# Kernel optimization log

Measured on AMD Instinct MI355X. Metric: run time of the kernel, lower is better.

The kernel has to match this reference:

```python
import jax, jax.numpy as jnp
import numpy as np

LAMBD = 0.05

def _mlp(y, W0, b0, W1, b1, W2, b2, W3, b3):
    h = jax.nn.relu(y @ W0.T + b0)
    h = jax.nn.relu(h @ W1.T + b1)
    h = jax.nn.relu(h @ W2.T + b2)
    return h @ W3.T + b3  # [N, 1]


def setup_inputs() -> dict:
    key = jax.random.key(0)
    ks = jax.random.split(key, 8)
    B, N, D = 4096, 20000, 784
    s = lambda fan_in: 1.0 / np.sqrt(fan_in)
    return {
        "x": jax.random.normal(ks[0], (B, D), jnp.float32),
        "y": jax.random.normal(ks[1], (N, D), jnp.float32),
        "nu": jax.random.uniform(ks[2], (N,), jnp.float32, 0.1, 1.0),
        "W0": jax.random.normal(ks[3], (512, D), jnp.float32) * s(D),
        "b0": jnp.zeros((512,), jnp.float32),
        "W1": jax.random.normal(ks[4], (256, 512), jnp.float32) * s(512),
        "b1": jnp.zeros((256,), jnp.float32),
        "W2": jax.random.normal(ks[5], (128, 256), jnp.float32) * s(256),
        "b2": jnp.zeros((128,), jnp.float32),
        "W3": jax.random.normal(ks[6], (1, 128), jnp.float32) * s(128),
        "b3": jnp.zeros((1,), jnp.float32),
    }


def reference(x, y, nu, W0, b0, W1, b1, W2, b2, W3, b3):
    # squared-distance cost matrix [B, N], normalized by mean(|y|^2)
    sy2 = jnp.sum(y * y, axis=1)            # [N]
    normalization = sy2.mean()
    cxy = (jnp.sum(x * x, axis=1, keepdims=True) + sy2[None, :]
           - 2.0 * (x @ y.T)) / normalization  # [B, N]
    psiy = _mlp(y, W0, b0, W1, b1, W2, b2, W3, b3)[:, 0]  # [N]
    # entropic semi-dual: -lambd * logsumexp((psi(y) - c(x,y))/lambd + log nu)
    z = (psiy[None, :] - cxy) / LAMBD + jnp.log(nu)[None, :]
    out = -LAMBD * jax.nn.logsumexp(z, axis=1) + psiy.mean()  # [B]
    return out
```

## Files before the change

### kernel.cpp

```cpp
#include <hip/hip_runtime.h>
#include <math.h>
#include <stdint.h>
#include <stddef.h>

#define B_ROWS 4096
#define N_REAL 20000
#define NP2    20224
#define NJT2   79
#define NRT    16
#define D_IN   784
#define DP2    800
#define NKS    25
#define NKT    13
#define YBLK   316
#define XBLK   64
#define PW     158
#define LAMBD  0.05f
#define LN2    0.69314718055994530942f
#define QS     (4.5f / 127.f)
#define QINV   (127.f / 4.5f)

typedef __attribute__((ext_vector_type(8))) short bf16x8;
typedef __attribute__((ext_vector_type(4))) float f32x4;
typedef __attribute__((ext_vector_type(4))) int   i32x4;

typedef const unsigned int __attribute__((address_space(1)))* gas_u32p;
typedef unsigned int __attribute__((address_space(3)))* las_u32p;

static __device__ __forceinline__ void gload_lds16(const void* g, void* l) {
  __builtin_amdgcn_global_load_lds((gas_u32p)g, (las_u32p)l, 16, 0, 0);
}

static __device__ __forceinline__ float bf2f(short s) {
  union { unsigned u; float f; } c;
  c.u = ((unsigned)(unsigned short)s) << 16;
  return c.f;
}
static __device__ __forceinline__ short f2bf(float f) {
  union { float f; unsigned u; } c;
  c.f = f;
  unsigned r = (c.u + 0x7fffu + ((c.u >> 16) & 1u)) >> 16;
  return (short)(unsigned short)r;
}
static __device__ __forceinline__ unsigned q4c(float a, float b, float c, float d) {
  int x0 = min(127, max(-127, (int)rintf(a * QINV))) & 255;
  int x1 = min(127, max(-127, (int)rintf(b * QINV))) & 255;
  int x2 = min(127, max(-127, (int)rintf(c * QINV))) & 255;
  int x3 = min(127, max(-127, (int)rintf(d * QINV))) & 255;
  return (unsigned)(x0 | (x1 << 8) | (x2 << 16) | (x3 << 24));
}

__global__ void k_prep(const float* __restrict__ ysrc, const float* __restrict__ xsrc,
                       unsigned char* __restrict__ y_i8, unsigned char* __restrict__ x_i8,
                       short* __restrict__ y_bf, float* __restrict__ sy2,
                       float* __restrict__ x2,
                       const float* __restrict__ W0, const float* __restrict__ W1,
                       const float* __restrict__ W2, short* __restrict__ W0b,
                       short* __restrict__ W1b, short* __restrict__ W2b,
                       unsigned* __restrict__ ctr) {
  const int b = blockIdx.x, t = threadIdx.x;
  if (b == 0 && t == 0) *ctr = 0u;

  if (b >= YBLK + XBLK) {
    const int wb_ = b - (YBLK + XBLK);
    const float* src; short* dst; int r, cs, cp;
    if (wb_ < 512)      { r = wb_;       src = W0; dst = W0b; cs = D_IN; cp = DP2; }
    else if (wb_ < 768) { r = wb_ - 512; src = W1; dst = W1b; cs = 512;  cp = 512; }
    else                { r = wb_ - 768; src = W2; dst = W2b; cs = 256;  cp = 256; }
    const float* sp = src + (size_t)r * cs;
    short* dp = dst + (size_t)r * cp;
    for (int c = t; c < cp; c += 256)
      dp[c] = f2bf(c < cs ? sp[c] : 0.f);
    return;
  }

  const float* src; unsigned char* di8; float* rowsum;
  int rows_real, g; bool wbf;
  if (b < YBLK) { src = ysrc; di8 = y_i8; rowsum = sy2;
                  rows_real = N_REAL; g = b; wbf = true; }
  else          { src = xsrc; di8 = x_i8; rowsum = x2;
                  rows_real = B_ROWS; g = b - YBLK; wbf = false; }
  const int q = t & 3, r = t >> 2;
  const int grow = g * 64 + r;
  const int tile1 = grow >> 8, sub1 = grow & 255;
  const float* sp = src + (size_t)grow * D_IN;
  const bool realRow = grow < rows_real;
  float sq = 0.f;

  for (int kt = 0; kt < NKT; ++kt) {
    const int c0 = kt * 64 + q * 16;
    float v[16];
    if (realRow && c0 < D_IN) {
      #pragma unroll
      for (int u = 0; u < 4; ++u) {
        float4 w4 = *(const float4*)(sp + c0 + u * 4);
        v[u*4+0] = w4.x; v[u*4+1] = w4.y; v[u*4+2] = w4.z; v[u*4+3] = w4.w;
        sq += w4.x * w4.x + w4.y * w4.y + w4.z * w4.z + w4.w * w4.w;
      }
    } else {
      #pragma unroll
      for (int e = 0; e < 16; ++e) v[e] = 0.f;
    }
    uint4 pk;
    pk.x = q4c(v[0],  v[1],  v[2],  v[3]);
    pk.y = q4c(v[4],  v[5],  v[6],  v[7]);
    pk.z = q4c(v[8],  v[9],  v[10], v[11]);
    pk.w = q4c(v[12], v[13], v[14], v[15]);
    *(uint4*)(di8 + (size_t)(tile1 * NKT + kt) * 16384
              + ((size_t)(q * 256 + sub1) << 4)) = pk;
    if (wbf) {
      const int ks = kt * 2 + (q >> 1);
      if (ks < NKS) {
        const int oct = (q & 1) * 2;
        short* dp = y_bf + (size_t)(tile1 * NKS + ks) * 8192
                  + ((size_t)(oct * 256 + sub1) << 3);
        bf16x8 o0, o1;
        #pragma unroll
        for (int e = 0; e < 8; ++e) { o0[e] = f2bf(v[e]); o1[e] = f2bf(v[8 + e]); }
        *(bf16x8*)dp = o0;
        *(bf16x8*)(dp + 2048) = o1;
      }
    }
  }

  sq += __shfl_xor(sq, 1, 4);
  sq += __shfl_xor(sq, 2, 4);
  if (q == 0 && realRow) rowsum[grow] = sq;
}

template <bool TA>
__global__ __launch_bounds__(256) void k_gemmf(const short* __restrict__ A,
                                               const short* __restrict__ Bm,
                                               const float* __restrict__ bias,
                                               short* __restrict__ C,
                                               int K, int Ncols,
                                               const float* __restrict__ sy2n,
                                               float* __restrict__ scaln) {
  extern __shared__ short L[];
  const int t = threadIdx.x;
  const int rb = blockIdx.y, cb = blockIdx.x;

  if (sy2n != nullptr && rb == NP2 / 128) {
    if (cb != 0) return;
    __shared__ float red[4];
    float a = 0.f;
    for (int j = t; j < N_REAL; j += 256) a += sy2n[j];
    #pragma unroll
    for (int m = 1; m < 64; m <<= 1) a += __shfl_xor(a, m, 64);
    if ((t & 63) == 0) red[t >> 6] = a;
    __syncthreads();
    if (t == 0) {
      float norm = (red[0] + red[1] + red[2] + red[3]) / (float)N_REAL;
      scaln[0] = norm;
      scaln[1] = 1.0f / norm;
      scaln[2] = 2.0f / (norm * LAMBD * LN2);
    }
    return;
  }

  const int lane = t & 63, wave = t >> 6;
  const int lr = lane & 15, lg = lane >> 4;
  const int wrow = (wave >> 1) * 64, wcol = (wave & 1) * 64;
  const int KS = K >> 5;
  const int wb = wave * 512;

  const int prow = t & 127, psel = t >> 7;
  const short* aS0; const short* aS1; int aStep;
  if constexpr (TA) {
    const short* base = A + (size_t)((rb >> 1) * NKS) * 8192
                      + ((size_t)((rb & 1) * 128 + prow) << 3);
    aS0 = base + (size_t)(psel * 2048);
    aS1 = base + (size_t)((2 + psel) * 2048);
    aStep = 8192;
  } else {
    const short* base = A + (size_t)(rb * 128 + prow) * K;
    aS0 = base + psel * 8;
    aS1 = base + (2 + psel) * 8;
    aStep = 32;
  }
  const short* bBase = Bm + (size_t)(cb * 128 + prow) * K;
  const short* bS0 = bBase + psel * 8;
  const short* bS1 = bBase + (2 + psel) * 8;

  auto stage = [&](int s) {
    short* Lb = L + (s % 3) * 8192;
    gload_lds16(aS0 + (size_t)s * aStep, Lb + wb);
    gload_lds16(aS1 + (size_t)s * aStep, Lb + 2048 + wb);
    gload_lds16(bS0 + (size_t)s * 32,    Lb + 4096 + wb);
    gload_lds16(bS1 + (size_t)s * 32,    Lb + 4096 + 2048 + wb);
  };

  f32x4 acc[4][4];
  #pragma unroll
  for (int mi = 0; mi < 4; ++mi)
    #pragma unroll
    for (int ni = 0; ni < 4; ++ni)
      acc[mi][ni] = (f32x4){0.f, 0.f, 0.f, 0.f};

  stage(0);
  stage(1);
  asm volatile("s_waitcnt vmcnt(4)" ::: "memory");
  __builtin_amdgcn_s_barrier();
  __builtin_amdgcn_sched_barrier(0);

  const int aro = (wrow + lr) * 8;
  const int bro = (wcol + lr) * 8;
  for (int ks = 0; ks < KS; ++ks) {
    if (ks + 2 < KS) stage(ks + 2);
    const short* LA = L + (ks % 3) * 8192 + lg * 1024;
    const short* LB = LA + 4096;
    bf16x8 b0 = *(const bf16x8*)&LB[bro];
    bf16x8 b1 = *(const bf16x8*)&LB[bro + 128];
    bf16x8 b2 = *(const bf16x8*)&LB[bro + 256];
    bf16x8 b3 = *(const bf16x8*)&LB[bro + 384];
    bf16x8 a0 = *(const bf16x8*)&LA[aro];
    bf16x8 a1 = *(const bf16x8*)&LA[aro + 128];
    bf16x8 a2v = *(const bf16x8*)&LA[aro + 256];
    bf16x8 a3v = *(const bf16x8*)&LA[aro + 384];
    __builtin_amdgcn_s_setprio(1);
    #pragma unroll
    for (int ni = 0; ni < 4; ++ni) {
      bf16x8 bv = ni == 0 ? b0 : ni == 1 ? b1 : ni == 2 ? b2 : b3;
      acc[0][ni] = __builtin_amdgcn_mfma_f32_16x16x32_bf16(a0, bv, acc[0][ni], 0, 0, 0);
      acc[1][ni] = __builtin_amdgcn_mfma_f32_16x16x32_bf16(a1, bv, acc[1][ni], 0, 0, 0);
      acc[2][ni] = __builtin_amdgcn_mfma_f32_16x16x32_bf16(a2v, bv, acc[2][ni], 0, 0, 0);
      acc[3][ni] = __builtin_amdgcn_mfma_f32_16x16x32_bf16(a3v, bv, acc[3][ni], 0, 0, 0);
    }
    __builtin_amdgcn_s_setprio(0);
    if (ks + 2 < KS) {
      asm volatile("s_waitcnt vmcnt(4)" ::: "memory");
      __builtin_amdgcn_s_barrier();
      __builtin_amdgcn_sched_barrier(0);
    } else if (ks + 1 < KS) {
      asm volatile("s_waitcnt vmcnt(0)" ::: "memory");
      __builtin_amdgcn_s_barrier();
      __builtin_amdgcn_sched_barrier(0);
    }
  }

  #pragma unroll
  for (int ni = 0; ni < 4; ++ni) {
    const int col = cb * 128 + wcol + ni * 16 + lr;
    const float bv = bias[col];
    #pragma unroll
    for (int mi = 0; mi < 4; ++mi) {
      const int row0 = rb * 128 + wrow + mi * 16 + lg * 4;
      #pragma unroll
      for (int r = 0; r < 4; ++r)
        C[(size_t)(row0 + r) * Ncols + col] = f2bf(fmaxf(acc[mi][ni][r] + bv, 0.f));
    }
  }
}

__global__ __launch_bounds__(256) void k_mlp12(const short* __restrict__ H1,
                                               const short* __restrict__ W1b,
                                               const float* __restrict__ b1,
                                               const short* __restrict__ W2b,
                                               const float* __restrict__ b2,
                                               const float* __restrict__ W3,
                                               const float* __restrict__ b3,
                                               float* __restrict__ psi) {
  extern __shared__ short L[];
  const int t = threadIdx.x;
  const int lane = t & 63, wave = t >> 6;
  const int lr = lane & 15, lg = lane >> 4;
  const int wr = wave >> 1, wc2 = wave & 1;
  const int rb = blockIdx.x;
  const int wb = wave * 512;

  float b1v[8], b2v[4], w3v[4];
  #pragma unroll
  for (int ni = 0; ni < 8; ++ni) b1v[ni] = b1[wc2 * 128 + ni * 16 + lr];
  #pragma unroll
  for (int ni = 0; ni < 4; ++ni) {
    b2v[ni] = b2[wc2 * 64 + ni * 16 + lr];
    w3v[ni] = W3[wc2 * 64 + ni * 16 + lr];
  }
  const float b3v = b3[0];

  const int prow = t & 127, psel = t >> 7;
  const short* aBase = H1 + (size_t)(rb * 128 + prow) * 512;
  const short* aS0 = aBase + psel * 8;
  const short* aS1 = aBase + (2 + psel) * 8;
  const int bcol = wave * 64 + lane;
  const short* bBase = W1b + (size_t)bcol * 512;

  auto stageA = [&](int s) {
    short* Lb = L + (s % 3) * 12288;
    gload_lds16(aS0 + s * 32, Lb + wb);
    gload_lds16(aS1 + s * 32, Lb + 2048 + wb);
    #pragma unroll
    for (int j = 0; j < 4; ++j)
      gload_lds16(bBase + s * 32 + j * 8, Lb + 4096 + j * 2048 + wb);
  };

  f32x4 acc[4][8];
  #pragma unroll
  for (int mi = 0; mi < 4; ++mi)
    #pragma unroll
    for (int ni = 0; ni < 8; ++ni)
      acc[mi][ni] = (f32x4){0.f, 0.f, 0.f, 0.f};

  stageA(0);
  stageA(1);
  asm volatile("s_waitcnt vmcnt(6)" ::: "memory");
  __builtin_amdgcn_s_barrier();
  __builtin_amdgcn_sched_barrier(0);

  const int aro = (wr * 64 + lr) * 8;
  const int bro = (wc2 * 128 + lr) * 8;
  for (int ks = 0; ks < 16; ++ks) {
    if (ks + 2 < 16) stageA(ks + 2);
    const short* LA = L + (ks % 3) * 12288 + lg * 1024;
    const short* LB = L + (ks % 3) * 12288 + 4096 + lg * 2048;
    bf16x8 af[4];
    #pragma unroll
    for (int mi = 0; mi < 4; ++mi)
      af[mi] = *(const bf16x8*)&LA[aro + mi * 128];
    bf16x8 bfr[8];
    #pragma unroll
    for (int ni = 0; ni < 8; ++ni)
      bfr[ni] = *(const bf16x8*)&LB[bro + ni * 128];
    __builtin_amdgcn_s_setprio(1);
    #pragma unroll
    for (int ni = 0; ni < 8; ++ni) {
      acc[0][ni] = __builtin_amdgcn_mfma_f32_16x16x32_bf16(af[0], bfr[ni], acc[0][ni], 0, 0, 0);
      acc[1][ni] = __builtin_amdgcn_mfma_f32_16x16x32_bf16(af[1], bfr[ni], acc[1][ni], 0, 0, 0);
      acc[2][ni] = __builtin_amdgcn_mfma_f32_16x16x32_bf16(af[2], bfr[ni], acc[2][ni], 0, 0, 0);
      acc[3][ni] = __builtin_amdgcn_mfma_f32_16x16x32_bf16(af[3], bfr[ni], acc[3][ni], 0, 0, 0);
    }
    __builtin_amdgcn_s_setprio(0);
    if (ks + 2 < 16) {
      asm volatile("s_waitcnt vmcnt(6)" ::: "memory");
      __builtin_amdgcn_s_barrier();
      __builtin_amdgcn_sched_barrier(0);
    } else if (ks + 1 < 16) {
      asm volatile("s_waitcnt vmcnt(0)" ::: "memory");
      __builtin_amdgcn_s_barrier();
      __builtin_amdgcn_sched_barrier(0);
    }
  }
  __syncthreads();

  #pragma unroll
  for (int j = 0; j < 16; ++j) {
    const int bbyte = j * 4096 + wave * 1024 + lane * 16;
    const int ks2 = bbyte >> 13, kc = (bbyte >> 11) & 3, row = (bbyte >> 4) & 127;
    gload_lds16(W2b + row * 256 + ks2 * 32 + kc * 8, L + j * 2048 + wb);
  }

  short* H2i = L + 36864;
  #pragma unroll
  for (int ni = 0; ni < 8; ++ni) {
    const int col = wc2 * 128 + ni * 16 + lr;
    const int ks2 = col >> 5, kc = (col >> 3) & 3, e = col & 7;
    const float bv = b1v[ni];
    #pragma unroll
    for (int mi = 0; mi < 4; ++mi)
      #pragma unroll
      for (int r = 0; r < 4; ++r) {
        const int row = wr * 64 + mi * 16 + lg * 4 + r;
        H2i[ks2 * 4096 + kc * 1024 + row * 8 + e] =
            f2bf(fmaxf(acc[mi][ni][r] + bv, 0.f));
      }
  }
  asm volatile("s_waitcnt vmcnt(0)" ::: "memory");
  __syncthreads();

  f32x4 acc2[4][4];
  #pragma unroll
  for (int mi = 0; mi < 4; ++mi)
    #pragma unroll
    for (int ni = 0; ni < 4; ++ni)
      acc2[mi][ni] = (f32x4){0.f, 0.f, 0.f, 0.f};
  const int aro2 = (wr * 64 + lr) * 8;
  const int bro2 = (wc2 * 64 + lr) * 8;
  #pragma unroll
  for (int ks = 0; ks < 8; ++ks) {
    const short* HA = H2i + ks * 4096 + lg * 1024;
    const short* WB = L + ks * 4096 + lg * 1024;
    bf16x8 af[4], bfr[4];
    #pragma unroll
    for (int mi = 0; mi < 4; ++mi) af[mi] = *(const bf16x8*)&HA[aro2 + mi * 128];
    #pragma unroll
    for (int ni = 0; ni < 4; ++ni) bfr[ni] = *(const bf16x8*)&WB[bro2 + ni * 128];
    #pragma unroll
    for (int mi = 0; mi < 4; ++mi)
      #pragma unroll
      for (int ni = 0; ni < 4; ++ni)
        acc2[mi][ni] = __builtin_amdgcn_mfma_f32_16x16x32_bf16(af[mi], bfr[ni], acc2[mi][ni], 0, 0, 0);
  }

  float part[4][4];
  #pragma unroll
  for (int mi = 0; mi < 4; ++mi)
    #pragma unroll
    for (int r = 0; r < 4; ++r) part[mi][r] = 0.f;
  #pragma unroll
  for (int ni = 0; ni < 4; ++ni) {
    #pragma unroll
    for (int mi = 0; mi < 4; ++mi)
      #pragma unroll
      for (int r = 0; r < 4; ++r)
        part[mi][r] += fmaxf(acc2[mi][ni][r] + b2v[ni], 0.f) * w3v[ni];
  }
  #pragma unroll
  for (int mi = 0; mi < 4; ++mi)
    #pragma unroll
    for (int r = 0; r < 4; ++r) {
      float s = part[mi][r];
      s += __shfl_xor(s, 1, 16);
      s += __shfl_xor(s, 2, 16);
      s += __shfl_xor(s, 4, 16);
      s += __shfl_xor(s, 8, 16);
      part[mi][r] = s;
    }
  __syncthreads();
  float* pbuf = (float*)L;
  if (lr == 0) {
    #pragma unroll
    for (int mi = 0; mi < 4; ++mi)
      #pragma unroll
      for (int r = 0; r < 4; ++r)
        pbuf[wc2 * 128 + wr * 64 + mi * 16 + lg * 4 + r] = part[mi][r];
  }
  __syncthreads();
  if (t < 128) psi[rb * 128 + t] = pbuf[t] + pbuf[t + 128] + b3v;
}

__global__ void k_a2(const float* __restrict__ psi, const float* __restrict__ sy2,
                     const float* __restrict__ nu, const float* __restrict__ scal,
                     float* __restrict__ a2raw, float* __restrict__ maxp,
                     float* __restrict__ sump, unsigned* __restrict__ ctr,
                     float* __restrict__ scalw) {
  const int j = blockIdx.x * 256 + threadIdx.x;
  const float invn = scal[1];
  float a = -1e30f, p = 0.f;
  if (j < NP2) {
    if (j < N_REAL) {
      p = psi[j];
      a = (p - sy2[j] * invn) * (1.0f / (LAMBD * LN2)) + log2f(nu[j]);
    }
    a2raw[j] = a;
  }
  __shared__ float redm[4], reds[4];
  __shared__ int lastFlag;
  #pragma unroll
  for (int m = 1; m < 64; m <<= 1) {
    a = fmaxf(a, __shfl_xor(a, m, 64));
    p += __shfl_xor(p, m, 64);
  }
  const int t = threadIdx.x;
  if ((t & 63) == 0) { redm[t >> 6] = a; reds[t >> 6] = p; }
  __syncthreads();
  if (t == 0) {
    maxp[blockIdx.x] = fmaxf(fmaxf(redm[0], redm[1]), fmaxf(redm[2], redm[3]));
    sump[blockIdx.x] = reds[0] + reds[1] + reds[2] + reds[3];
    __threadfence();
    lastFlag = (atomicAdd(ctr, 1u) == (unsigned)(gridDim.x - 1));
  }
  __syncthreads();
  if (lastFlag) {
    __threadfence();
    float am = -1e30f, s = 0.f;
    for (int i = t; i < (int)gridDim.x; i += 256) {
      am = fmaxf(am, maxp[i]);
      s += sump[i];
    }
    #pragma unroll
    for (int m = 1; m < 64; m <<= 1) {
      am = fmaxf(am, __shfl_xor(am, m, 64));
      s += __shfl_xor(s, m, 64);
    }
    if ((t & 63) == 0) { redm[t >> 6] = am; reds[t >> 6] = s; }
    __syncthreads();
    if (t == 0) {
      scalw[3] = fmaxf(fmaxf(redm[0], redm[1]), fmaxf(redm[2], redm[3]));
      scalw[4] = (reds[0] + reds[1] + reds[2] + reds[3]) / (float)N_REAL;
    }
  }
}

__global__ __launch_bounds__(512, 2) void k_flash(const unsigned char* __restrict__ x_t,
                                                  const unsigned char* __restrict__ y_t,
                                                  const float* __restrict__ a2raw,
                                                  const float* __restrict__ scal,
                                                  float* __restrict__ parts) {
  extern __shared__ char Lsh[];
  const int t = threadIdx.x;
  const int lane = t & 63, wave = t >> 6;
  const int lr = lane & 15, lg = lane >> 4;
  const int wr = wave >> 1, wc = wave & 1;
  const int rbt = blockIdx.x, jt = blockIdx.y;

  const float s2c1 = QS * QS * scal[2];
  const float A2 = scal[3];

  const int t16 = t * 16;
  const int wb = wave * 1024;
  const int aoff = (lg * 256 + wr * 64 + lr) * 16;
  const int boff = (lg * 256 + wc * 128 + lr) * 16;

  const unsigned char* As = x_t + (size_t)(rbt * NKT) * 16384 + t16;
  const unsigned char* Bs = y_t + (size_t)(jt * NKT) * 16384 + t16;

  i32x4 acc[4][8];
  #pragma unroll
  for (int mi = 0; mi < 4; ++mi)
    #pragma unroll
    for (int ni = 0; ni < 8; ++ni)
      acc[mi][ni] = (i32x4){0, 0, 0, 0};

  auto stage = [&](int s) {
    char* Lb = Lsh + (s % 3) * 32768;
    const unsigned char* An = As + (size_t)s * 16384;
    const unsigned char* Bn = Bs + (size_t)s * 16384;
    gload_lds16(An,         Lb + wb);
    gload_lds16(An + 8192,  Lb + 8192 + wb);
    gload_lds16(Bn,         Lb + 16384 + wb);
    gload_lds16(Bn + 8192,  Lb + 24576 + wb);
  };

  stage(0);
  stage(1);
  asm volatile("s_waitcnt vmcnt(4)" ::: "memory");
  __builtin_amdgcn_s_barrier();
  __builtin_amdgcn_sched_barrier(0);

  #pragma unroll
  for (int ks = 0; ks < NKT; ++ks) {
    if (ks + 2 < NKT) stage(ks + 2);
    const char* LA = Lsh + (ks % 3) * 32768;
    const char* LB = LA + 16384;
    i32x4 bf[8];
    #pragma unroll
    for (int ni = 0; ni < 8; ++ni)
      bf[ni] = *(const i32x4*)(LB + boff + ni * 256);
    i32x4 af[4];
    #pragma unroll
    for (int mi = 0; mi < 4; ++mi)
      af[mi] = *(const i32x4*)(LA + aoff + mi * 256);
    __builtin_amdgcn_s_setprio(1);
    #pragma unroll
    for (int ni = 0; ni < 8; ++ni) {
      acc[0][ni] = __builtin_amdgcn_mfma_i32_16x16x64_i8(af[0], bf[ni], acc[0][ni], 0, 0, 0);
      acc[1][ni] = __builtin_amdgcn_mfma_i32_16x16x64_i8(af[1], bf[ni], acc[1][ni], 0, 0, 0);
      acc[2][ni] = __builtin_amdgcn_mfma_i32_16x16x64_i8(af[2], bf[ni], acc[2][ni], 0, 0, 0);
      acc[3][ni] = __builtin_amdgcn_mfma_i32_16x16x64_i8(af[3], bf[ni], acc[3][ni], 0, 0, 0);
    }
    __builtin_amdgcn_s_setprio(0);
    if (ks + 2 < NKT) {
      asm volatile("s_waitcnt vmcnt(4)" ::: "memory");
      __builtin_amdgcn_s_barrier();
      __builtin_amdgcn_sched_barrier(0);
    } else if (ks + 1 < NKT) {
      asm volatile("s_waitcnt vmcnt(0)" ::: "memory");
      __builtin_amdgcn_s_barrier();
      __builtin_amdgcn_sched_barrier(0);
    }
  }

  const int colb = jt * 256 + wc * 128 + lr;
  float av[8];
  #pragma unroll
  for (int ni = 0; ni < 8; ++ni)
    av[ni] = a2raw[colb + ni * 16] - A2;
  #pragma unroll
  for (int mi = 0; mi < 4; ++mi)
    #pragma unroll
    for (int r = 0; r < 4; ++r) {
      const int row = rbt * 256 + wr * 64 + mi * 16 + lg * 4 + r;
      float s = 0.f;
      #pragma unroll
      for (int ni = 0; ni < 8; ++ni)
        s += exp2f((float)acc[mi][ni][r] * s2c1 + av[ni]);
      s += __shfl_xor(s, 1, 16);
      s += __shfl_xor(s, 2, 16);
      s += __shfl_xor(s, 4, 16);
      s += __shfl_xor(s, 8, 16);
      if (lr == 0)
        parts[(size_t)row * PW + jt * 2 + wc] = s;
    }
}

__global__ void k_comb(const float* __restrict__ parts, const float* __restrict__ x2,
                       const float* __restrict__ scal, float* __restrict__ out) {
  const int wave = threadIdx.x >> 6, lane = threadIdx.x & 63;
  const int row = blockIdx.x * 4 + wave;
  const float* pr = parts + (size_t)row * PW;
  float s = 0.f;
  for (int i = lane; i < PW; i += 64) s += pr[i];
  #pragma unroll
  for (int m = 1; m < 64; m <<= 1) s += __shfl_xor(s, m, 64);
  if (lane == 0)
    out[row] = -(LAMBD * LN2) * (scal[3] + log2f(s)) + x2[row] * scal[1] + scal[4];
}

extern "C" void kernel_launch(void* const* d_in, const int* in_sizes, int n_in,
                              void* d_out, int out_size, void* d_ws, size_t ws_size,
                              hipStream_t stream) {
  const float* x  = (const float*)d_in[0];
  const float* y  = (const float*)d_in[1];
  const float* nu = (const float*)d_in[2];
  const float* W0 = (const float*)d_in[3];
  const float* b0 = (const float*)d_in[4];
  const float* W1 = (const float*)d_in[5];
  const float* b1 = (const float*)d_in[6];
  const float* W2 = (const float*)d_in[7];
  const float* b2 = (const float*)d_in[8];
  const float* W3 = (const float*)d_in[9];
  const float* b3 = (const float*)d_in[10];
  float* out = (float*)d_out;

  char* w = (char*)d_ws;
  auto alloc = [&](size_t bytes) {
    char* p = w;
    w += (bytes + 255) & ~(size_t)255;
    return p;
  };
  unsigned char* y_i8 = (unsigned char*)alloc((size_t)NJT2 * NKT * 16384);
  unsigned char* x_i8 = (unsigned char*)alloc((size_t)NRT * NKT * 16384);
  short* y_bf  = (short*)alloc((size_t)(NP2 / 256) * NKS * 8192 * 2);
  short* W0b   = (short*)alloc((size_t)512 * DP2 * 2);
  short* W1b   = (short*)alloc((size_t)256 * 512 * 2);
  short* W2b   = (short*)alloc((size_t)128 * 256 * 2);
  short* H1    = (short*)alloc((size_t)NP2 * 512 * 2);
  float* sy2   = (float*)alloc((size_t)N_REAL * 4);
  float* x2    = (float*)alloc((size_t)B_ROWS * 4);
  float* psi   = (float*)alloc((size_t)NP2 * 4);
  float* a2raw = (float*)alloc((size_t)NP2 * 4);
  float* maxp  = (float*)alloc(128 * 4);
  float* sump  = (float*)alloc(128 * 4);
  float* scal  = (float*)alloc(64 * 4);
  unsigned* ctr = (unsigned*)alloc(256);
  float* parts = (float*)alloc((size_t)B_ROWS * PW * 4);

  k_prep<<<dim3(YBLK + XBLK + 896), dim3(256), 0, stream>>>(y, x, y_i8, x_i8, y_bf,
                                                            sy2, x2, W0, W1, W2,
                                                            W0b, W1b, W2b, ctr);

  hipFuncSetAttribute((const void*)k_gemmf<true>, hipFuncAttributeMaxDynamicSharedMemorySize, 49152);
  k_gemmf<true><<<dim3(4, NP2 / 128 + 1), dim3(256), 49152, stream>>>(
      y_bf, W0b, b0, H1, DP2, 512, sy2, scal);

  hipFuncSetAttribute((const void*)k_mlp12, hipFuncAttributeMaxDynamicSharedMemorySize, 139264);
  k_mlp12<<<dim3(NP2 / 128), dim3(256), 139264, stream>>>(H1, W1b, b1, W2b, b2, W3, b3, psi);

  k_a2<<<dim3(NP2 / 256), dim3(256), 0, stream>>>(psi, sy2, nu, scal, a2raw,
                                                  maxp, sump, ctr, scal);

  hipFuncSetAttribute((const void*)k_flash, hipFuncAttributeMaxDynamicSharedMemorySize, 98304);
  k_flash<<<dim3(NRT, NJT2), dim3(512), 98304, stream>>>(x_i8, y_i8, a2raw, scal, parts);
  k_comb<<<dim3(B_ROWS / 4), dim3(256), 0, stream>>>(parts, x2, scal, out);
}
```

Before: 173.5 us.

## Restructure int8 flash GEMM into 2x4 wave tiling with interleaved quarter-tile prefetch

Changes the k_flash wave layout from 4x2 to 2x4, so each wave computes 128 rows by 64 columns, and reorganises the int8 tile layout in LDS into half-tiles. The main loop is split into four phases, each issuing one quarter of the next prefetch and one batch of MFMAs, separated by barriers. This aims to overlap global-to-LDS loads with MFMA work at a finer grain and to reduce the LDS fragment loads per phase. The partial-sum width doubles because each block now writes four column groups, and launch bounds drop to one block per CU, which trades occupancy for register room and adds many barriers.

```diff
diff --git a/kernel.cpp b/kernel.cpp
--- a/kernel.cpp
+++ b/kernel.cpp
@@ -14,7 +14,7 @@
 #define NKT    13
 #define YBLK   316
 #define XBLK   64
-#define PW     158
+#define PW     316
 #define LAMBD  0.05f
 #define LN2    0.69314718055994530942f
 #define QS     (4.5f / 127.f)
@@ -107,7 +107,8 @@
     pk.z = q4c(v[8],  v[9],  v[10], v[11]);
     pk.w = q4c(v[12], v[13], v[14], v[15]);
     *(uint4*)(di8 + (size_t)(tile1 * NKT + kt) * 16384
-              + ((size_t)(q * 256 + sub1) << 4)) = pk;
+              + (size_t)((sub1 >> 7) * 8192)
+              + ((size_t)((q << 7) + (sub1 & 127)) << 4)) = pk;
     if (wbf) {
       const int ks = kt * 2 + (q >> 1);
       if (ks < NKS) {
@@ -481,7 +482,7 @@
   }
 }
 
-__global__ __launch_bounds__(512, 2) void k_flash(const unsigned char* __restrict__ x_t,
+__global__ __launch_bounds__(512, 1) void k_flash(const unsigned char* __restrict__ x_t,
                                                   const unsigned char* __restrict__ y_t,
                                                   const float* __restrict__ a2raw,
                                                   const float* __restrict__ scal,
@@ -490,96 +491,156 @@
   const int t = threadIdx.x;
   const int lane = t & 63, wave = t >> 6;
   const int lr = lane & 15, lg = lane >> 4;
-  const int wr = wave >> 1, wc = wave & 1;
+  const int wr = wave >> 2, wc = wave & 3;
   const int rbt = blockIdx.x, jt = blockIdx.y;
 
   const float s2c1 = QS * QS * scal[2];
   const float A2 = scal[3];
 
   const int t16 = t * 16;
-  const int wb = wave * 1024;
-  const int aoff = (lg * 256 + wr * 64 + lr) * 16;
-  const int boff = (lg * 256 + wc * 128 + lr) * 16;
+  const int wvb = wave * 1024;
+  const int aoff = (lg * 128 + lr) * 16;
+  const int boff = (lg * 128 + (wc & 1) * 64 + lr) * 16;
+  const int ahalf = wr;
+  const int bhalf = wc >> 1;
 
   const unsigned char* As = x_t + (size_t)(rbt * NKT) * 16384 + t16;
   const unsigned char* Bs = y_t + (size_t)(jt * NKT) * 16384 + t16;
 
-  i32x4 acc[4][8];
-  #pragma unroll
-  for (int mi = 0; mi < 4; ++mi)
-    #pragma unroll
-    for (int ni = 0; ni < 8; ++ni)
+  i32x4 acc[8][4];
+  #pragma unroll
+  for (int mi = 0; mi < 8; ++mi)
+    #pragma unroll
+    for (int ni = 0; ni < 4; ++ni)
       acc[mi][ni] = (i32x4){0, 0, 0, 0};
 
-  auto stage = [&](int s) {
-    char* Lb = Lsh + (s % 3) * 32768;
-    const unsigned char* An = As + (size_t)s * 16384;
-    const unsigned char* Bn = Bs + (size_t)s * 16384;
-    gload_lds16(An,         Lb + wb);
-    gload_lds16(An + 8192,  Lb + 8192 + wb);
-    gload_lds16(Bn,         Lb + 16384 + wb);
-    gload_lds16(Bn + 8192,  Lb + 24576 + wb);
+  auto issue = [&](int m, int h) {
+    const int slot = (4 * m + h) % 12;
+    const unsigned char* src = (h < 2 ? As : Bs) + (size_t)m * 16384 + (h & 1) * 8192;
+    gload_lds16(src, Lsh + slot * 8192 + wvb);
   };
 
-  stage(0);
-  stage(1);
+  #pragma unroll
+  for (int h = 0; h < 4; ++h) issue(0, h);
+  #pragma unroll
+  for (int h = 0; h < 4; ++h) issue(1, h);
   asm volatile("s_waitcnt vmcnt(4)" ::: "memory");
   __builtin_amdgcn_s_barrier();
   __builtin_amdgcn_sched_barrier(0);
 
-  #pragma unroll
-  for (int ks = 0; ks < NKT; ++ks) {
-    if (ks + 2 < NKT) stage(ks + 2);
-    const char* LA = Lsh + (ks % 3) * 32768;
-    const char* LB = LA + 16384;
-    i32x4 bf[8];
-    #pragma unroll
-    for (int ni = 0; ni < 8; ++ni)
-      bf[ni] = *(const i32x4*)(LB + boff + ni * 256);
-    i32x4 af[4];
-    #pragma unroll
-    for (int mi = 0; mi < 4; ++mi)
-      af[mi] = *(const i32x4*)(LA + aoff + mi * 256);
+  for (int m = 0; m < NKT; ++m) {
+    const int sb = ((4 * m) % 12) * 8192;
+    const char* LA = Lsh + sb + ahalf * 8192 + aoff;
+    const char* LB = Lsh + sb + 16384 + bhalf * 8192 + boff;
+    const bool pf = (m + 2 < NKT);
+    i32x4 fa0, fa1, fa2, fa3, fa4, fa5, fa6, fa7, fb0, fb1, fb2, fb3;
+
+    fa0 = *(const i32x4*)(LA);
+    fa1 = *(const i32x4*)(LA + 256);
+    fa2 = *(const i32x4*)(LA + 512);
+    fa3 = *(const i32x4*)(LA + 768);
+    fb0 = *(const i32x4*)(LB);
+    fb1 = *(const i32x4*)(LB + 256);
+    if (pf) issue(m + 2, 0);
+    __builtin_amdgcn_sched_barrier(0);
+    __builtin_amdgcn_s_barrier();
+    asm volatile("s_waitcnt lgkmcnt(0)" ::: "memory");
+    __builtin_amdgcn_sched_barrier(0);
     __builtin_amdgcn_s_setprio(1);
-    #pragma unroll
-    for (int ni = 0; ni < 8; ++ni) {
-      acc[0][ni] = __builtin_amdgcn_mfma_i32_16x16x64_i8(af[0], bf[ni], acc[0][ni], 0, 0, 0);
-      acc[1][ni] = __builtin_amdgcn_mfma_i32_16x16x64_i8(af[1], bf[ni], acc[1][ni], 0, 0, 0);
-      acc[2][ni] = __builtin_amdgcn_mfma_i32_16x16x64_i8(af[2], bf[ni], acc[2][ni], 0, 0, 0);
-      acc[3][ni] = __builtin_amdgcn_mfma_i32_16x16x64_i8(af[3], bf[ni], acc[3][ni], 0, 0, 0);
-    }
+    acc[0][0] = __builtin_amdgcn_mfma_i32_16x16x64_i8(fa0, fb0, acc[0][0], 0, 0, 0);
+    acc[1][0] = __builtin_amdgcn_mfma_i32_16x16x64_i8(fa1, fb0, acc[1][0], 0, 0, 0);
+    acc[2][0] = __builtin_amdgcn_mfma_i32_16x16x64_i8(fa2, fb0, acc[2][0], 0, 0, 0);
+    acc[3][0] = __builtin_amdgcn_mfma_i32_16x16x64_i8(fa3, fb0, acc[3][0], 0, 0, 0);
+    acc[0][1] = __builtin_amdgcn_mfma_i32_16x16x64_i8(fa0, fb1, acc[0][1], 0, 0, 0);
+    acc[1][1] = __builtin_amdgcn_mfma_i32_16x16x64_i8(fa1, fb1, acc[1][1], 0, 0, 0);
+    acc[2][1] = __builtin_amdgcn_mfma_i32_16x16x64_i8(fa2, fb1, acc[2][1], 0, 0, 0);
+    acc[3][1] = __builtin_amdgcn_mfma_i32_16x16x64_i8(fa3, fb1, acc[3][1], 0, 0, 0);
     __builtin_amdgcn_s_setprio(0);
-    if (ks + 2 < NKT) {
-      asm volatile("s_waitcnt vmcnt(4)" ::: "memory");
+    __builtin_amdgcn_s_barrier();
+    __builtin_amdgcn_sched_barrier(0);
+
+    fb2 = *(const i32x4*)(LB + 512);
+    fb3 = *(const i32x4*)(LB + 768);
+    if (pf) issue(m + 2, 1);
+    __builtin_amdgcn_sched_barrier(0);
+    __builtin_amdgcn_s_barrier();
+    asm volatile("s_waitcnt lgkmcnt(0)" ::: "memory");
+    __builtin_amdgcn_sched_barrier(0);
+    __builtin_amdgcn_s_setprio(1);
+    acc[0][2] = __builtin_amdgcn_mfma_i32_16x16x64_i8(fa0, fb2, acc[0][2], 0, 0, 0);
+    acc[1][2] = __builtin_amdgcn_mfma_i32_16x16x64_i8(fa1, fb2, acc[1][2], 0, 0, 0);
+    acc[2][2] = __builtin_amdgcn_mfma_i32_16x16x64_i8(fa2, fb2, acc[2][2], 0, 0, 0);
+    acc[3][2] = __builtin_amdgcn_mfma_i32_16x16x64_i8(fa3, fb2, acc[3][2], 0, 0, 0);
+    acc[0][3] = __builtin_amdgcn_mfma_i32_16x16x64_i8(fa0, fb3, acc[0][3], 0, 0, 0);
+    acc[1][3] = __builtin_amdgcn_mfma_i32_16x16x64_i8(fa1, fb3, acc[1][3], 0, 0, 0);
+    acc[2][3] = __builtin_amdgcn_mfma_i32_16x16x64_i8(fa2, fb3, acc[2][3], 0, 0, 0);
+    acc[3][3] = __builtin_amdgcn_mfma_i32_16x16x64_i8(fa3, fb3, acc[3][3], 0, 0, 0);
+    __builtin_amdgcn_s_setprio(0);
+    __builtin_amdgcn_s_barrier();
+    __builtin_amdgcn_sched_barrier(0);
+
+    fa4 = *(const i32x4*)(LA + 1024);
+    fa5 = *(const i32x4*)(LA + 1280);
+    fa6 = *(const i32x4*)(LA + 1536);
+    fa7 = *(const i32x4*)(LA + 1792);
+    if (pf) issue(m + 2, 2);
+    __builtin_amdgcn_sched_barrier(0);
+    __builtin_amdgcn_s_barrier();
+    asm volatile("s_waitcnt lgkmcnt(0)" ::: "memory");
+    __builtin_amdgcn_sched_barrier(0);
+    __builtin_amdgcn_s_setprio(1);
+    acc[4][0] = __builtin_amdgcn_mfma_i32_16x16x64_i8(fa4, fb0, acc[4][0], 0, 0, 0);
+    acc[5][0] = __builtin_amdgcn_mfma_i32_16x16x64_i8(fa5, fb0, acc[5][0], 0, 0, 0);
+    acc[6][0] = __builtin_amdgcn_mfma_i32_16x16x64_i8(fa6, fb0, acc[6][0], 0, 0, 0);
+    acc[7][0] = __builtin_amdgcn_mfma_i32_16x16x64_i8(fa7, fb0, acc[7][0], 0, 0, 0);
+    acc[4][1] = __builtin_amdgcn_mfma_i32_16x16x64_i8(fa4, fb1, acc[4][1], 0, 0, 0);
+    acc[5][1] = __builtin_amdgcn_mfma_i32_16x16x64_i8(fa5, fb1, acc[5][1], 0, 0, 0);
+    acc[6][1] = __builtin_amdgcn_mfma_i32_16x16x64_i8(fa6, fb1, acc[6][1], 0, 0, 0);
+    acc[7][1] = __builtin_amdgcn_mfma_i32_16x16x64_i8(fa7, fb1, acc[7][1], 0, 0, 0);
+    __builtin_amdgcn_s_setprio(0);
+    __builtin_amdgcn_s_barrier();
+    __builtin_amdgcn_sched_barrier(0);
+
+    if (pf) issue(m + 2, 3);
+    __builtin_amdgcn_sched_barrier(0);
+    __builtin_amdgcn_s_setprio(1);
+    acc[4][2] = __builtin_amdgcn_mfma_i32_16x16x64_i8(fa4, fb2, acc[4][2], 0, 0, 0);
+    acc[5][2] = __builtin_amdgcn_mfma_i32_16x16x64_i8(fa5, fb2, acc[5][2], 0, 0, 0);
+    acc[6][2] = __builtin_amdgcn_mfma_i32_16x16x64_i8(fa6, fb2, acc[6][2], 0, 0, 0);
+    acc[7][2] = __builtin_amdgcn_mfma_i32_16x16x64_i8(fa7, fb2, acc[7][2], 0, 0, 0);
+    acc[4][3] = __builtin_amdgcn_mfma_i32_16x16x64_i8(fa4, fb3, acc[4][3], 0, 0, 0);
+    acc[5][3] = __builtin_amdgcn_mfma_i32_16x16x64_i8(fa5, fb3, acc[5][3], 0, 0, 0);
+    acc[6][3] = __builtin_amdgcn_mfma_i32_16x16x64_i8(fa6, fb3, acc[6][3], 0, 0, 0);
+    acc[7][3] = __builtin_amdgcn_mfma_i32_16x16x64_i8(fa7, fb3, acc[7][3], 0, 0, 0);
+    __builtin_amdgcn_s_setprio(0);
+    if (m + 1 < NKT) {
+      if (pf) asm volatile("s_waitcnt vmcnt(4)" ::: "memory");
+      else    asm volatile("s_waitcnt vmcnt(0)" ::: "memory");
       __builtin_amdgcn_s_barrier();
       __builtin_amdgcn_sched_barrier(0);
-    } else if (ks + 1 < NKT) {
-      asm volatile("s_waitcnt vmcnt(0)" ::: "memory");
-      __builtin_amdgcn_s_barrier();
-      __builtin_amdgcn_sched_barrier(0);
-    }
-  }
-
-  const int colb = jt * 256 + wc * 128 + lr;
-  float av[8];
-  #pragma unroll
-  for (int ni = 0; ni < 8; ++ni)
+    }
+  }
+
+  const int colb = jt * 256 + wc * 64 + lr;
+  float av[4];
+  #pragma unroll
+  for (int ni = 0; ni < 4; ++ni)
     av[ni] = a2raw[colb + ni * 16] - A2;
   #pragma unroll
-  for (int mi = 0; mi < 4; ++mi)
+  for (int mi = 0; mi < 8; ++mi)
     #pragma unroll
     for (int r = 0; r < 4; ++r) {
-      const int row = rbt * 256 + wr * 64 + mi * 16 + lg * 4 + r;
-      float s = 0.f;
-      #pragma unroll
-      for (int ni = 0; ni < 8; ++ni)
-        s += exp2f((float)acc[mi][ni][r] * s2c1 + av[ni]);
+      const int row = rbt * 256 + wr * 128 + mi * 16 + lg * 4 + r;
+      float s = exp2f((float)acc[mi][0][r] * s2c1 + av[0])
+              + exp2f((float)acc[mi][1][r] * s2c1 + av[1])
+              + exp2f((float)acc[mi][2][r] * s2c1 + av[2])
+              + exp2f((float)acc[mi][3][r] * s2c1 + av[3]);
       s += __shfl_xor(s, 1, 16);
       s += __shfl_xor(s, 2, 16);
       s += __shfl_xor(s, 4, 16);
       s += __shfl_xor(s, 8, 16);
       if (lr == 0)
-        parts[(size_t)row * PW + jt * 2 + wc] = s;
+        parts[(size_t)row * PW + jt * 4 + wc] = s;
     }
 }
 
```

After: 182.9 us. 1.05x slower.
